# Kernel optimization log

Hardware: AMD Instinct MI355X
Metric: run time of the kernel (lower is better)

Reference implementation:

```python
import jax, jax.numpy as jnp
import numpy as np

EPS = 1e-5

def _ln(x, w, b):
    m = jnp.mean(x, axis=-1, keepdims=True)
    d = x - m
    v = jnp.mean(d * d, axis=-1, keepdims=True)
    return d * jax.lax.rsqrt(v + EPS) * w + b

def setup_inputs() -> dict:
    key = jax.random.key(0)
    ks = jax.random.split(key, 8)
    B, N, C, H = 4, 1024, 1024, 16
    D = C // H
    Hid = 4 * C
    s = 0.02
    return {
        "x": jax.random.normal(ks[0], (B, N, C), jnp.float32),
        "rel_bias": jax.random.normal(ks[1], (H, N, N), jnp.float32) * 0.02,
        "qkv_w": jax.random.normal(ks[2], (3 * C, C), jnp.float32) * s,
        "qnorm_w": jnp.ones((D,), jnp.float32), "qnorm_b": jnp.zeros((D,), jnp.float32),
        "knorm_w": jnp.ones((D,), jnp.float32), "knorm_b": jnp.zeros((D,), jnp.float32),
        "proj_w": jax.random.normal(ks[3], (C, C), jnp.float32) * s,
        "proj_b": jnp.zeros((C,), jnp.float32),
        "norm1_w": jnp.ones((C,), jnp.float32), "norm1_b": jnp.zeros((C,), jnp.float32),
        "norm2_w": jnp.ones((C,), jnp.float32), "norm2_b": jnp.zeros((C,), jnp.float32),
        "fc1_w": jax.random.normal(ks[4], (Hid, C), jnp.float32) * s,
        "fc1_b": jnp.zeros((Hid,), jnp.float32),
        "fc2_w": jax.random.normal(ks[5], (C, Hid), jnp.float32) * s,
        "fc2_b": jnp.zeros((C,), jnp.float32),
        "ls1_gamma": jnp.full((C,), 1e-5, jnp.float32),
        "ls2_gamma": jnp.full((C,), 1e-5, jnp.float32),
    }

def reference(x, rel_bias, qkv_w, qnorm_w, qnorm_b, knorm_w, knorm_b,
              proj_w, proj_b, norm1_w, norm1_b, norm2_w, norm2_b,
              fc1_w, fc1_b, fc2_w, fc2_b, ls1_gamma, ls2_gamma):
    B, N, C = x.shape
    H = rel_bias.shape[0]
    D = C // H
    scale = D ** -0.5
    # --- attention branch ---
    h = _ln(x, norm1_w, norm1_b)
    qkv = (h @ qkv_w.T).reshape(B, N, 3, H, D).transpose(2, 0, 3, 1, 4)  # [3,B,H,N,D]
    q, k, v = qkv[0], qkv[1], qkv[2]
    q = _ln(q, qnorm_w, qnorm_b)  # per-head QK LayerNorm on head_dim
    k = _ln(k, knorm_w, knorm_b)
    attn = jnp.einsum('bhnd,bhmd->bhnm', q * scale, k) + rel_bias[None]  # rel-pos bias
    attn = jax.nn.softmax(attn, axis=-1)
    o = jnp.einsum('bhnm,bhmd->bhnd', attn, v).transpose(0, 2, 1, 3).reshape(B, N, C)
    o = o @ proj_w.T + proj_b
    x = x + ls1_gamma * o  # LayerScale + residual (droppath inactive in eval)
    # --- MLP branch ---
    h2 = _ln(x, norm2_w, norm2_b)
    m = jax.nn.gelu(h2 @ fc1_w.T + fc1_b, approximate=False) @ fc2_w.T + fc2_b
    return x + ls2_gamma * m
```

## Files before the change

kernel.cpp:

```cpp
#include <hip/hip_runtime.h>
#include <hip/hip_bf16.h>


typedef __attribute__((ext_vector_type(8))) short short8;
typedef __attribute__((ext_vector_type(4))) float f32x4;

#define MFMA16(a, b, c) __builtin_amdgcn_mfma_f32_16x16x32_bf16(a, b, c, 0, 0, 0)

static __device__ __forceinline__ unsigned short f2b(float f) {
  union { __hip_bfloat16 h; unsigned short u; } cv;
  cv.h = __float2bfloat16(f);
  return cv.u;
}

static __device__ __forceinline__ void gld16(const unsigned short* g,
                                             unsigned short* l) {
  __builtin_amdgcn_global_load_lds(
      (const __attribute__((address_space(1))) void*)g,
      (__attribute__((address_space(3))) void*)l, 16, 0, 0);
}

static __device__ __forceinline__ void drain_dma_then_barrier() {
  asm volatile("s_waitcnt vmcnt(0)" ::: "memory");
  __builtin_amdgcn_sched_barrier(0);
  __syncthreads();
}

__global__ void cvt_bf16_kernel(const float* __restrict__ in,
                                unsigned short* __restrict__ out, int n4) {
  int i = blockIdx.x * blockDim.x + threadIdx.x;
  int stride = gridDim.x * blockDim.x;
  for (; i < n4; i += stride) {
    float4 v = reinterpret_cast<const float4*>(in)[i];
    ushort4 o;
    o.x = f2b(v.x); o.y = f2b(v.y); o.z = f2b(v.z); o.w = f2b(v.w);
    reinterpret_cast<ushort4*>(out)[i] = o;
  }
}

__global__ __launch_bounds__(256) void ln_kernel(const float* __restrict__ x,
                                                 const float* __restrict__ w,
                                                 const float* __restrict__ b,
                                                 unsigned short* __restrict__ out) {
  int row = blockIdx.x, tid = threadIdx.x;
  const float* xr = x + (size_t)row * 1024;
  float4 v = reinterpret_cast<const float4*>(xr)[tid];
  float s = v.x + v.y + v.z + v.w;
  float s2 = v.x * v.x + v.y * v.y + v.z * v.z + v.w * v.w;
  for (int off = 1; off < 64; off <<= 1) {
    s += __shfl_xor(s, off);
    s2 += __shfl_xor(s2, off);
  }
  __shared__ float red[8];
  int wid = tid >> 6;
  if ((tid & 63) == 0) { red[wid] = s; red[4 + wid] = s2; }
  __syncthreads();
  s = red[0] + red[1] + red[2] + red[3];
  s2 = red[4] + red[5] + red[6] + red[7];
  float mean = s * (1.f / 1024.f);
  float rs = rsqrtf(s2 * (1.f / 1024.f) - mean * mean + 1e-5f);
  float4 wv = reinterpret_cast<const float4*>(w)[tid];
  float4 bv = reinterpret_cast<const float4*>(b)[tid];
  ushort4 o;
  o.x = f2b((v.x - mean) * rs * wv.x + bv.x);
  o.y = f2b((v.y - mean) * rs * wv.y + bv.y);
  o.z = f2b((v.z - mean) * rs * wv.z + bv.z);
  o.w = f2b((v.w - mean) * rs * wv.w + bv.w);
  reinterpret_cast<ushort4*>(out + (size_t)row * 1024)[tid] = o;
}

__global__ __launch_bounds__(256) void qkpack_kernel(
    const float* __restrict__ qkv, const float* __restrict__ qw,
    const float* __restrict__ qb, const float* __restrict__ kw,
    const float* __restrict__ kb_, unsigned short* __restrict__ Q,
    unsigned short* __restrict__ K, unsigned short* __restrict__ Vt) {
  int wid = blockIdx.x * 4 + (threadIdx.x >> 6);
  int lane = threadIdx.x & 63;
  int m = wid >> 4;
  int h = wid & 15;
  int b = m >> 10, n = m & 1023;
  const float* base = qkv + (size_t)m * 3072 + h * 64 + lane;
  float q = base[0], k = base[1024], v = base[2048];
  float qs = q, qs2 = q * q, ks = k, ks2 = k * k;
  for (int off = 1; off < 64; off <<= 1) {
    qs += __shfl_xor(qs, off); qs2 += __shfl_xor(qs2, off);
    ks += __shfl_xor(ks, off); ks2 += __shfl_xor(ks2, off);
  }
  float qm = qs * (1.f / 64.f), qv = qs2 * (1.f / 64.f) - qm * qm;
  float km = ks * (1.f / 64.f), kv = ks2 * (1.f / 64.f) - km * km;
  float qn = (q - qm) * rsqrtf(qv + 1e-5f) * qw[lane] + qb[lane];
  float kn = (k - km) * rsqrtf(kv + 1e-5f) * kw[lane] + kb_[lane];
  int bh = b * 16 + h;
  Q[((size_t)bh * 1024 + n) * 64 + lane] = f2b(qn * 0.125f);
  K[((size_t)bh * 1024 + n) * 64 + lane] = f2b(kn);
  Vt[((size_t)bh * 64 + lane) * 1024 + n] = f2b(v);
}

__global__ __launch_bounds__(256) void attn_kernel(
    const unsigned short* __restrict__ Q, const unsigned short* __restrict__ K,
    const unsigned short* __restrict__ Vt, const float* __restrict__ rb,
    unsigned short* __restrict__ O) {
  __shared__ unsigned short Ks[32][80];
  __shared__ unsigned short Vs[64][40];
  __shared__ unsigned short Ps[4][16][40];
  int bid = blockIdx.x;
  int qt = bid & 15, bh = bid >> 4;
  int h = bh & 15, b = bh >> 4;
  int q0 = qt * 64;
  int tid = threadIdx.x, lane = tid & 63, w = tid >> 6;
  int lg = lane >> 4, lr = lane & 15;

  short8 qf[2];
  {
    int qrow = q0 + w * 16 + lr;
    const unsigned short* qp = Q + ((size_t)bh * 1024 + qrow) * 64;
    qf[0] = *reinterpret_cast<const short8*>(qp + lg * 8);
    qf[1] = *reinterpret_cast<const short8*>(qp + 32 + lg * 8);
  }
  f32x4 o[4] = {};
  float mrow[4], lrow[4];
  for (int i = 0; i < 4; i++) { mrow[i] = -1e30f; lrow[i] = 0.f; }
  const float* rbh = rb + (size_t)h * 1024 * 1024;

  for (int kt = 0; kt < 32; kt++) {
    __syncthreads();
    {
      int r = tid >> 3, c = (tid & 7) * 8;
      *reinterpret_cast<short8*>(&Ks[r][c]) =
          *reinterpret_cast<const short8*>(K + ((size_t)bh * 1024 + kt * 32 + r) * 64 + c);
      int d = tid >> 2, j = (tid & 3) * 8;
      *reinterpret_cast<short8*>(&Vs[d][j]) =
          *reinterpret_cast<const short8*>(Vt + ((size_t)bh * 64 + d) * 1024 + kt * 32 + j);
    }
    __syncthreads();
    f32x4 s[2] = {};
    for (int t = 0; t < 2; t++) {
      short8 kf0 = *reinterpret_cast<const short8*>(&Ks[t * 16 + lr][lg * 8]);
      short8 kf1 = *reinterpret_cast<const short8*>(&Ks[t * 16 + lr][32 + lg * 8]);
      s[t] = MFMA16(qf[0], kf0, s[t]);
      s[t] = MFMA16(qf[1], kf1, s[t]);
    }
    int myrow = q0 + w * 16 + lg * 4;
    for (int i = 0; i < 4; i++) {
      float s0 = s[0][i] + rbh[(size_t)(myrow + i) * 1024 + kt * 32 + lr];
      float s1 = s[1][i] + rbh[(size_t)(myrow + i) * 1024 + kt * 32 + 16 + lr];
      float mx = fmaxf(s0, s1);
      for (int off = 1; off < 16; off <<= 1) mx = fmaxf(mx, __shfl_xor(mx, off));
      float mnew = fmaxf(mrow[i], mx);
      float corr = __expf(mrow[i] - mnew);
      float p0 = __expf(s0 - mnew), p1 = __expf(s1 - mnew);
      float ps = p0 + p1;
      for (int off = 1; off < 16; off <<= 1) ps += __shfl_xor(ps, off);
      lrow[i] = lrow[i] * corr + ps;
      mrow[i] = mnew;
      for (int nd = 0; nd < 4; nd++) o[nd][i] *= corr;
      Ps[w][lg * 4 + i][lr] = f2b(p0);
      Ps[w][lg * 4 + i][16 + lr] = f2b(p1);
    }
    __syncthreads();
    short8 pa = *reinterpret_cast<const short8*>(&Ps[w][lr][lg * 8]);
    for (int nd = 0; nd < 4; nd++) {
      short8 vf = *reinterpret_cast<const short8*>(&Vs[nd * 16 + lr][lg * 8]);
      o[nd] = MFMA16(pa, vf, o[nd]);
    }
  }
  for (int i = 0; i < 4; i++) {
    float inv = 1.f / lrow[i];
    int n = q0 + w * 16 + lg * 4 + i;
    size_t base = ((size_t)(b * 1024 + n)) * 1024 + h * 64;
    for (int nd = 0; nd < 4; nd++) O[base + nd * 16 + lr] = f2b(o[nd][i] * inv);
  }
}

template <int MODE, int BM>
__global__ __launch_bounds__(256) void gemm_bt(
    const unsigned short* __restrict__ A, const unsigned short* __restrict__ W,
    const float* __restrict__ bias, const float* __restrict__ resid,
    const float* __restrict__ gamma, float* __restrict__ outF,
    unsigned short* __restrict__ outB, int M, int Nn, int Kd) {
  constexpr int BN = 128;
  constexpr int MI = BM / 32;
  constexpr int ACH = BM / 16;
  constexpr int TCH = ACH + BN / 16;
  constexpr int CPW = TCH / 4;
  __shared__ unsigned short S[2][(BM + BN) * 32];
  int tid = threadIdx.x;
  int lane = tid & 63, wv = tid >> 6;
  int wm = wv >> 1, wn = wv & 1;
  int lg = lane >> 4, lr = lane & 15;
  int nbx = Nn >> 7;
  int cpx = gridDim.x >> 3;
  int swz = (blockIdx.x & 7) * cpx + (blockIdx.x >> 3);
  int m0 = (swz / nbx) * BM, n0 = (swz % nbx) * BN;
  f32x4 acc[MI][4] = {};
  int lrow = lane >> 2;
  int lcol = (lane & 3) * 8;
  const unsigned short* gbase[CPW];
#pragma unroll
  for (int i = 0; i < CPW; i++) {
    int c = wv + i * 4;
    gbase[i] = (c < ACH)
        ? A + (size_t)(m0 + c * 16 + lrow) * Kd + lcol
        : W + (size_t)(n0 + (c - ACH) * 16 + lrow) * Kd + lcol;
  }
  auto stage = [&](int buf, int k0) {
#pragma unroll
    for (int i = 0; i < CPW; i++) {
      int c = wv + i * 4;
      gld16(gbase[i] + k0, &S[buf][c * 512]);
    }
  };
  stage(0, 0);
  drain_dma_then_barrier();
  int cur = 0;
  for (int k0 = 0; k0 < Kd; k0 += 32) {
    int nxt = cur ^ 1;
    if (k0 + 32 < Kd) stage(nxt, k0 + 32);
    const unsigned short* Sa = &S[cur][0];
    const unsigned short* Sb = &S[cur][BM * 32];
    short8 af[MI], bf[4];
#pragma unroll
    for (int i = 0; i < MI; i++)
      af[i] = *reinterpret_cast<const short8*>(
          &Sa[(wm * (BM / 2) + i * 16 + lr) * 32 + lg * 8]);
#pragma unroll
    for (int i = 0; i < 4; i++)
      bf[i] = *reinterpret_cast<const short8*>(
          &Sb[(wn * 64 + i * 16 + lr) * 32 + lg * 8]);
#pragma unroll
    for (int mi = 0; mi < MI; mi++)
#pragma unroll
      for (int ni = 0; ni < 4; ni++)
        acc[mi][ni] = MFMA16(af[mi], bf[ni], acc[mi][ni]);
    drain_dma_then_barrier();
    cur = nxt;
  }
  int row0 = m0 + wm * (BM / 2), col0 = n0 + wn * 64;
#pragma unroll
  for (int mi = 0; mi < MI; mi++)
#pragma unroll
    for (int ni = 0; ni < 4; ni++) {
      int col = col0 + ni * 16 + lr;
      int rbase = row0 + mi * 16 + lg * 4;
      for (int i = 0; i < 4; i++) {
        int row = rbase + i;
        float v = acc[mi][ni][i];
        if (MODE == 0) {
          outF[(size_t)row * Nn + col] = v;
        } else if (MODE == 1) {
          outF[(size_t)row * Nn + col] =
              resid[(size_t)row * Nn + col] + gamma[col] * (v + bias[col]);
        } else {
          float t = v + bias[col];
          float g = 0.5f * t * (1.f + erff(t * 0.70710678f));
          outB[(size_t)row * Nn + col] = f2b(g);
        }
      }
    }
}

extern "C" void kernel_launch(void* const* d_in, const int* in_sizes, int n_in,
                              void* d_out, int out_size, void* d_ws, size_t ws_size,
                              hipStream_t stream) {
  const float* x      = (const float*)d_in[0];
  const float* relb   = (const float*)d_in[1];
  const float* qkv_w  = (const float*)d_in[2];
  const float* qnw    = (const float*)d_in[3];
  const float* qnb    = (const float*)d_in[4];
  const float* knw    = (const float*)d_in[5];
  const float* knb    = (const float*)d_in[6];
  const float* proj_w = (const float*)d_in[7];
  const float* proj_b = (const float*)d_in[8];
  const float* n1w    = (const float*)d_in[9];
  const float* n1b    = (const float*)d_in[10];
  const float* n2w    = (const float*)d_in[11];
  const float* n2b    = (const float*)d_in[12];
  const float* fc1_w  = (const float*)d_in[13];
  const float* fc1_b  = (const float*)d_in[14];
  const float* fc2_w  = (const float*)d_in[15];
  const float* fc2_b  = (const float*)d_in[16];
  const float* ls1    = (const float*)d_in[17];
  const float* ls2    = (const float*)d_in[18];
  float* out = (float*)d_out;

  char* ws = (char*)d_ws;
  size_t off = 0;
  auto take = [&](size_t bytes) {
    char* p = ws + off;
    off += (bytes + 255) & ~(size_t)255;
    return p;
  };
  unsigned short* h     = (unsigned short*)take((size_t)4096 * 1024 * 2);
  unsigned short* wqkv  = (unsigned short*)take((size_t)3072 * 1024 * 2);
  unsigned short* wproj = (unsigned short*)take((size_t)1024 * 1024 * 2);
  unsigned short* wfc1  = (unsigned short*)take((size_t)4096 * 1024 * 2);
  unsigned short* wfc2  = (unsigned short*)take((size_t)4096 * 1024 * 2);
  float*          qkvb  = (float*)take((size_t)4096 * 3072 * 4);
  unsigned short* Q     = (unsigned short*)take((size_t)64 * 1024 * 64 * 2);
  unsigned short* Kb    = (unsigned short*)take((size_t)64 * 1024 * 64 * 2);
  unsigned short* Vt    = (unsigned short*)take((size_t)64 * 64 * 1024 * 2);
  unsigned short* ao    = (unsigned short*)take((size_t)4096 * 1024 * 2);
  float*          x1    = (float*)take((size_t)4096 * 1024 * 4);
  unsigned short* h2 = h;
  unsigned short* m1 = (unsigned short*)qkvb;

  cvt_bf16_kernel<<<1024, 256, 0, stream>>>(qkv_w, wqkv, 3072 * 1024 / 4);
  cvt_bf16_kernel<<<1024, 256, 0, stream>>>(proj_w, wproj, 1024 * 1024 / 4);
  cvt_bf16_kernel<<<1024, 256, 0, stream>>>(fc1_w, wfc1, 4096 * 1024 / 4);
  cvt_bf16_kernel<<<1024, 256, 0, stream>>>(fc2_w, wfc2, 4096 * 1024 / 4);

  ln_kernel<<<4096, 256, 0, stream>>>(x, n1w, n1b, h);
  gemm_bt<0, 128><<<768, 256, 0, stream>>>(h, wqkv, nullptr, nullptr, nullptr,
                                           qkvb, nullptr, 4096, 3072, 1024);
  qkpack_kernel<<<16384, 256, 0, stream>>>(qkvb, qnw, qnb, knw, knb, Q, Kb, Vt);
  attn_kernel<<<1024, 256, 0, stream>>>(Q, Kb, Vt, relb, ao);
  gemm_bt<1, 64><<<512, 256, 0, stream>>>(ao, wproj, proj_b, x, ls1, x1,
                                          nullptr, 4096, 1024, 1024);
  ln_kernel<<<4096, 256, 0, stream>>>(x1, n2w, n2b, h2);
  gemm_bt<2, 128><<<1024, 256, 0, stream>>>(h2, wfc1, fc1_b, nullptr, nullptr,
                                            nullptr, m1, 4096, 4096, 1024);
  gemm_bt<1, 64><<<512, 256, 0, stream>>>(m1, wfc2, fc2_b, x1, ls2, out,
                                          nullptr, 4096, 1024, 4096);
}
```

Baseline: 475.8 us.

## Prefetch K/V tiles and rel-bias into registers, defer row-sum reduction

Result: faster. 446.2 us (-6.2%).

```diff
diff --git a/kernel.cpp b/kernel.cpp
--- a/kernel.cpp
+++ b/kernel.cpp
@@ -100,7 +100,7 @@
     const unsigned short* __restrict__ Q, const unsigned short* __restrict__ K,
     const unsigned short* __restrict__ Vt, const float* __restrict__ rb,
     unsigned short* __restrict__ O) {
-  __shared__ unsigned short Ks[32][80];
+  __shared__ unsigned short Ks[32][72];
   __shared__ unsigned short Vs[64][40];
   __shared__ unsigned short Ps[4][16][40];
   int bid = blockIdx.x;
@@ -118,40 +118,60 @@
     qf[1] = *reinterpret_cast<const short8*>(qp + 32 + lg * 8);
   }
   f32x4 o[4] = {};
-  float mrow[4], lrow[4];
-  for (int i = 0; i < 4; i++) { mrow[i] = -1e30f; lrow[i] = 0.f; }
+  float mrow[4], lsum[4];
+  for (int i = 0; i < 4; i++) { mrow[i] = -1e30f; lsum[i] = 0.f; }
   const float* rbh = rb + (size_t)h * 1024 * 1024;
+  int myrow = q0 + w * 16 + lg * 4;
+
+  int kr = tid >> 3, kc = (tid & 7) * 8;
+  int vd = tid >> 2, vj = (tid & 3) * 8;
+  const unsigned short* Kbase = K + ((size_t)bh * 1024 + kr) * 64 + kc;
+  const unsigned short* Vbase = Vt + ((size_t)bh * 64 + vd) * 1024 + vj;
+  short8 kreg = *reinterpret_cast<const short8*>(Kbase);
+  short8 vreg = *reinterpret_cast<const short8*>(Vbase);
+  float bpf[8];
+#pragma unroll
+  for (int i = 0; i < 4; i++) {
+    const float* bp = rbh + (size_t)(myrow + i) * 1024 + lr;
+    bpf[i] = bp[0];
+    bpf[4 + i] = bp[16];
+  }
 
   for (int kt = 0; kt < 32; kt++) {
+    int ktn = kt < 31 ? kt + 1 : 31;
     __syncthreads();
-    {
-      int r = tid >> 3, c = (tid & 7) * 8;
-      *reinterpret_cast<short8*>(&Ks[r][c]) =
-          *reinterpret_cast<const short8*>(K + ((size_t)bh * 1024 + kt * 32 + r) * 64 + c);
-      int d = tid >> 2, j = (tid & 3) * 8;
-      *reinterpret_cast<short8*>(&Vs[d][j]) =
-          *reinterpret_cast<const short8*>(Vt + ((size_t)bh * 64 + d) * 1024 + kt * 32 + j);
-    }
+    *reinterpret_cast<short8*>(&Ks[kr][kc]) = kreg;
+    *reinterpret_cast<short8*>(&Vs[vd][vj]) = vreg;
+    kreg = *reinterpret_cast<const short8*>(Kbase + (size_t)ktn * 2048);
+    vreg = *reinterpret_cast<const short8*>(Vbase + ktn * 32);
     __syncthreads();
+    float bcur[8];
+#pragma unroll
+    for (int i = 0; i < 8; i++) bcur[i] = bpf[i];
+#pragma unroll
+    for (int i = 0; i < 4; i++) {
+      const float* bp = rbh + (size_t)(myrow + i) * 1024 + ktn * 32 + lr;
+      bpf[i] = bp[0];
+      bpf[4 + i] = bp[16];
+    }
     f32x4 s[2] = {};
+#pragma unroll
     for (int t = 0; t < 2; t++) {
       short8 kf0 = *reinterpret_cast<const short8*>(&Ks[t * 16 + lr][lg * 8]);
       short8 kf1 = *reinterpret_cast<const short8*>(&Ks[t * 16 + lr][32 + lg * 8]);
       s[t] = MFMA16(qf[0], kf0, s[t]);
       s[t] = MFMA16(qf[1], kf1, s[t]);
     }
-    int myrow = q0 + w * 16 + lg * 4;
+#pragma unroll
     for (int i = 0; i < 4; i++) {
-      float s0 = s[0][i] + rbh[(size_t)(myrow + i) * 1024 + kt * 32 + lr];
-      float s1 = s[1][i] + rbh[(size_t)(myrow + i) * 1024 + kt * 32 + 16 + lr];
+      float s0 = s[0][i] + bcur[i];
+      float s1 = s[1][i] + bcur[4 + i];
       float mx = fmaxf(s0, s1);
       for (int off = 1; off < 16; off <<= 1) mx = fmaxf(mx, __shfl_xor(mx, off));
       float mnew = fmaxf(mrow[i], mx);
       float corr = __expf(mrow[i] - mnew);
       float p0 = __expf(s0 - mnew), p1 = __expf(s1 - mnew);
-      float ps = p0 + p1;
-      for (int off = 1; off < 16; off <<= 1) ps += __shfl_xor(ps, off);
-      lrow[i] = lrow[i] * corr + ps;
+      lsum[i] = lsum[i] * corr + p0 + p1;
       mrow[i] = mnew;
       for (int nd = 0; nd < 4; nd++) o[nd][i] *= corr;
       Ps[w][lg * 4 + i][lr] = f2b(p0);
@@ -159,13 +179,21 @@
     }
     __syncthreads();
     short8 pa = *reinterpret_cast<const short8*>(&Ps[w][lr][lg * 8]);
+#pragma unroll
     for (int nd = 0; nd < 4; nd++) {
       short8 vf = *reinterpret_cast<const short8*>(&Vs[nd * 16 + lr][lg * 8]);
       o[nd] = MFMA16(pa, vf, o[nd]);
     }
   }
+#pragma unroll
   for (int i = 0; i < 4; i++) {
-    float inv = 1.f / lrow[i];
+    float t = lsum[i];
+    for (int off = 1; off < 16; off <<= 1) t += __shfl_xor(t, off);
+    lsum[i] = t;
+  }
+#pragma unroll
+  for (int i = 0; i < 4; i++) {
+    float inv = 1.f / lsum[i];
     int n = q0 + w * 16 + lg * 4 + i;
     size_t base = ((size_t)(b * 1024 + n)) * 1024 + h * 64;
     for (int nd = 0; nd < 4; nd++) O[base + nd * 16 + lr] = f2b(o[nd][i] * inv);
```
